# Kernel optimization log

Hardware: AMD Instinct MI355X
Metric: run time of the kernel (lower is better)

The kernel has to match this reference:

```python
import jax, jax.numpy as jnp
import numpy as np
import math

D, H, DK, DFF, B, T, K = 512, 8, 64, 2048, 8, 512, 31
P = 2 * T - 1  # rel-pos length


def _ln(x, g, b, eps=1e-5):
    mu = jnp.mean(x, -1, keepdims=True)
    var = jnp.var(x, -1, keepdims=True)
    return (x - mu) * jax.lax.rsqrt(var + eps) * g + b


def _silu(x):
    return x * jax.nn.sigmoid(x)


def _rel_shift(x):
    # x: [B,H,T,P] -> NeMo-style relative shift
    b, h, t, p = x.shape
    x = jnp.pad(x, ((0, 0), (0, 0), (0, 0), (1, 0)))
    x = x.reshape(b, h, p + 1, t)
    return x[:, :, 1:, :].reshape(b, h, t, p)


def _forward(x, pos_emb, ln1_g, ln1_b, ff1_w1, ff1_b1, ff1_w2, ff1_b2,
             lna_g, lna_b, wq, bq, wk, bk, wv, bv, wo, bo, wpos, pbu, pbv,
             lnc_g, lnc_b, pw1_w, pw1_b, dw_w, dw_b, cln_g, cln_b, pw2_w, pw2_b,
             ln2_g, ln2_b, ff2_w1, ff2_b1, ff2_w2, ff2_b2, lno_g, lno_b):
    b, t, d = x.shape
    h, dk = pbu.shape
    # FF1 (half-step residual)
    r = x
    y = _ln(x, ln1_g, ln1_b)
    y = _silu(y @ ff1_w1 + ff1_b1) @ ff1_w2 + ff1_b2
    r = r + 0.5 * y
    # Rel-pos multi-head attention
    y = _ln(r, lna_g, lna_b)
    q = (y @ wq + bq).reshape(b, t, h, dk)
    k = (y @ wk + bk).reshape(b, t, h, dk)
    v = (y @ wv + bv).reshape(b, t, h, dk)
    p = (pos_emb @ wpos).reshape(pos_emb.shape[0], -1, h, dk)[0]  # [P,H,dk]
    ac = jnp.einsum('bthd,bshd->bhts', q + pbu, k)
    bd = jnp.einsum('bthd,phd->bhtp', q + pbv, p)
    bd = _rel_shift(bd)[..., :t]
    attn = jax.nn.softmax((ac + bd) / math.sqrt(dk), axis=-1)
    o = jnp.einsum('bhts,bshd->bthd', attn, v).reshape(b, t, d) @ wo + bo
    r = r + o
    # Conformer convolution module (layer_norm variant)
    y = _ln(r, lnc_g, lnc_b)
    y = y @ pw1_w + pw1_b                       # [B,T,2D] pointwise conv1
    a, g = jnp.split(y, 2, axis=-1)
    y = a * jax.nn.sigmoid(g)                   # GLU over channels
    y = jnp.transpose(y, (0, 2, 1))             # [B,D,T]
    pad = (dw_w.shape[1] - 1) // 2
    y = jax.lax.conv_general_dilated(
        y, dw_w[:, None, :], (1,), [(pad, pad)],
        feature_group_count=d, dimension_numbers=('NCH', 'OIH', 'NCH'))
    y = y + dw_b[None, :, None]
    y = jnp.transpose(y, (0, 2, 1))             # [B,T,D]
    y = _ln(y, cln_g, cln_b)
    y = _silu(y) @ pw2_w + pw2_b                # pointwise conv2
    r = r + y
    # FF2 (half-step residual)
    y = _ln(r, ln2_g, ln2_b)
    y = _silu(y @ ff2_w1 + ff2_b1) @ ff2_w2 + ff2_b2
    r = r + 0.5 * y
    return _ln(r, lno_g, lno_b)


def setup_inputs() -> dict:
    key = jax.random.key(0)
    ks = iter(jax.random.split(key, 64))
    rn = lambda shape, s=0.05: jax.random.normal(next(ks), shape, dtype=jnp.float32) * s
    ones = lambda n: jnp.ones((n,), jnp.float32)
    zeros = lambda n: jnp.zeros((n,), jnp.float32)
    return dict(
        x=jax.random.normal(next(ks), (B, T, D), jnp.float32),
        pos_emb=jax.random.normal(next(ks), (1, P, D), jnp.float32),
        ln1_g=ones(D), ln1_b=zeros(D),
        ff1_w1=rn((D, DFF)), ff1_b1=zeros(DFF), ff1_w2=rn((DFF, D)), ff1_b2=zeros(D),
        lna_g=ones(D), lna_b=zeros(D),
        wq=rn((D, D)), bq=zeros(D), wk=rn((D, D)), bk=zeros(D),
        wv=rn((D, D)), bv=zeros(D), wo=rn((D, D)), bo=zeros(D),
        wpos=rn((D, D)), pbu=rn((H, DK)), pbv=rn((H, DK)),
        lnc_g=ones(D), lnc_b=zeros(D),
        pw1_w=rn((D, 2 * D)), pw1_b=zeros(2 * D),
        dw_w=rn((D, K)), dw_b=zeros(D),
        cln_g=ones(D), cln_b=zeros(D),
        pw2_w=rn((D, D)), pw2_b=zeros(D),
        ln2_g=ones(D), ln2_b=zeros(D),
        ff2_w1=rn((D, DFF)), ff2_b1=zeros(DFF), ff2_w2=rn((DFF, D)), ff2_b2=zeros(D),
        lno_g=ones(D), lno_b=zeros(D))


def reference(x, pos_emb, ln1_g, ln1_b, ff1_w1, ff1_b1, ff1_w2, ff1_b2,
              lna_g, lna_b, wq, bq, wk, bk, wv, bv, wo, bo, wpos, pbu, pbv,
              lnc_g, lnc_b, pw1_w, pw1_b, dw_w, dw_b, cln_g, cln_b, pw2_w, pw2_b,
              ln2_g, ln2_b, ff2_w1, ff2_b1, ff2_w2, ff2_b2, lno_g, lno_b):
    return _forward(x, pos_emb, ln1_g, ln1_b, ff1_w1, ff1_b1, ff1_w2, ff1_b2,
                    lna_g, lna_b, wq, bq, wk, bk, wv, bv, wo, bo, wpos, pbu, pbv,
                    lnc_g, lnc_b, pw1_w, pw1_b, dw_w, dw_b, cln_g, cln_b, pw2_w, pw2_b,
                    ln2_g, ln2_b, ff2_w1, ff2_b1, ff2_w2, ff2_b2, lno_g, lno_b)
```

## Files before the change

kernel.cpp:

```cpp
#include <hip/hip_runtime.h>
#include <hip/hip_bf16.h>

#define Bb 8
#define Tt 512
#define Dd 512
#define Hh 8
#define DKk 64
#define DFFf 2048
#define Pp 1023
#define KCc 31
#define BTt 4096
#define QS 1536

typedef __hip_bfloat16 bf16;
typedef __attribute__((ext_vector_type(8))) short short8;
typedef __attribute__((ext_vector_type(4))) short s4v;
typedef __attribute__((ext_vector_type(4))) float f32x4;

union BFU { __hip_bfloat16 h; short s; };
static __device__ __forceinline__ short bfbits(float f) {
    BFU u; u.h = __float2bfloat16(f); return u.s;
}
static __device__ __forceinline__ float bff(short s) {
    BFU u; u.s = s; return __bfloat162float(u.h);
}
static __device__ __forceinline__ unsigned pk2(float a, float b) {
    return (unsigned)(unsigned short)bfbits(a) | ((unsigned)(unsigned short)bfbits(b) << 16);
}

static __device__ __forceinline__ int dflag(const void* lg) {
    return ((const unsigned*)lg)[0] == 0x3F803F80u;
}

#define GLD16(g, l) __builtin_amdgcn_global_load_lds(                          \
    (const __attribute__((address_space(1))) void*)(g),                        \
    (__attribute__((address_space(3))) void*)(l), 16, 0, 0)

struct CvtDesc { const void* src; unsigned n; unsigned off; unsigned startBlk; };
struct CvtArgs { CvtDesc d[32]; };

__global__ __launch_bounds__(256) void cvt_batch_k(CvtArgs args, int ncv,
                                                   bf16* __restrict__ dst,
                                                   const void* __restrict__ lg) {
    int bid = blockIdx.x;
    int ti = 0;
    while (ti + 1 < ncv && bid >= (int)args.d[ti + 1].startBlk) ti++;
    CvtDesc de = args.d[ti];
    unsigned i = (bid - de.startBlk) * 256u + threadIdx.x;
    if (i >= de.n) return;
    float v;
    if (dflag(lg)) v = __bfloat162float(((const bf16*)de.src)[i]);
    else           v = ((const float*)de.src)[i];
    dst[de.off + i] = __float2bfloat16(v);
}

struct TD { const void* src; unsigned doff, R, C, startBlk; };
struct TArgs { TD d[11]; };

__global__ __launch_bounds__(256) void transpose_batch_k(TArgs ta, bf16* __restrict__ wt,
                                                         const void* __restrict__ lg) {
    int bid = blockIdx.x;
    int ti = 0;
    while (ti + 1 < 11 && bid >= (int)ta.d[ti + 1].startBlk) ti++;
    TD t = ta.d[ti];
    int tile = bid - t.startBlk;
    int ntc = t.C >> 5;
    int tr = tile / ntc, tc = tile % ntc;
    __shared__ short tl[32][33];
    short* out = (short*)wt + t.doff;
    int tx = threadIdx.x & 31, ty = threadIdx.x >> 5;
    int fl = dflag(lg);
#pragma unroll
    for (int i = 0; i < 32; i += 8) {
        size_t idx = (size_t)(tr * 32 + ty + i) * t.C + tc * 32 + tx;
        short v;
        if (fl) v = ((const short*)t.src)[idx];
        else    v = bfbits(((const float*)t.src)[idx]);
        tl[ty + i][tx] = v;
    }
    __syncthreads();
#pragma unroll
    for (int i = 0; i < 32; i += 8)
        out[(size_t)(tc * 32 + ty + i) * t.R + tr * 32 + tx] = tl[tx][ty + i];
}

__global__ __launch_bounds__(256) void prep_misc_k(const void* __restrict__ dww, bf16* __restrict__ dwT,
                                                   const void* __restrict__ bq, const void* __restrict__ bk,
                                                   const void* __restrict__ bv, bf16* __restrict__ bqkv,
                                                   const void* __restrict__ lg) {
    int i = blockIdx.x * 256 + threadIdx.x;
    int fl = dflag(lg);
    if (i < Dd * KCc) {
        int d = i / KCc, j = i % KCc;
        short v = fl ? ((const short*)dww)[i] : bfbits(((const float*)dww)[i]);
        ((short*)dwT)[j * Dd + d] = v;
    } else {
        int j = i - Dd * KCc;
        if (j < QS) {
            const void* s = (j < 512) ? bq : ((j < 1024) ? bk : bv);
            int idx = j & 511;
            short v = fl ? ((const short*)s)[idx] : bfbits(((const float*)s)[idx]);
            ((short*)bqkv)[j] = v;
        }
    }
}

template <int SILU>
__global__ __launch_bounds__(256) void ln_k(const float* __restrict__ in,
                                            const bf16* __restrict__ g,
                                            const bf16* __restrict__ b,
                                            bf16* __restrict__ out) {
    int row = blockIdx.x;
    int tid = threadIdx.x;
    float2 v = ((const float2*)(in + (size_t)row * Dd))[tid];
    float s = v.x + v.y;
    float ss = v.x * v.x + v.y * v.y;
#pragma unroll
    for (int off = 32; off > 0; off >>= 1) {
        s += __shfl_xor(s, off);
        ss += __shfl_xor(ss, off);
    }
    __shared__ float red[2][4];
    int wid = tid >> 6;
    if ((tid & 63) == 0) { red[0][wid] = s; red[1][wid] = ss; }
    __syncthreads();
    float S = red[0][0] + red[0][1] + red[0][2] + red[0][3];
    float SS = red[1][0] + red[1][1] + red[1][2] + red[1][3];
    float mean = S * (1.0f / Dd);
    float var = SS * (1.0f / Dd) - mean * mean;
    float rstd = rsqrtf(var + 1e-5f);
    unsigned gp = *(const unsigned*)((const short*)g + 2 * tid);
    unsigned bp = *(const unsigned*)((const short*)b + 2 * tid);
    float o0 = (v.x - mean) * rstd * bff((short)(gp & 0xFFFF)) + bff((short)(bp & 0xFFFF));
    float o1 = (v.y - mean) * rstd * bff((short)(gp >> 16)) + bff((short)(bp >> 16));
    if (SILU) {
        o0 = o0 / (1.0f + __expf(-o0));
        o1 = o1 / (1.0f + __expf(-o1));
    }
    *(unsigned*)((short*)out + (size_t)row * Dd + 2 * tid) = pk2(o0, o1);
}

__global__ __launch_bounds__(256) void ln_x_k(const void* __restrict__ x,
                                              const bf16* __restrict__ g,
                                              const bf16* __restrict__ b,
                                              float* __restrict__ r,
                                              bf16* __restrict__ out,
                                              const void* __restrict__ lg) {
    int row = blockIdx.x;
    int tid = threadIdx.x;
    size_t base = (size_t)row * Dd;
    float v0, v1;
    if (dflag(lg)) {
        unsigned xp = *(const unsigned*)((const short*)x + base + 2 * tid);
        v0 = bff((short)(xp & 0xFFFF));
        v1 = bff((short)(xp >> 16));
    } else {
        float2 xv = ((const float2*)((const float*)x + base))[tid];
        v0 = xv.x; v1 = xv.y;
    }
    ((float2*)(r + base))[tid] = make_float2(v0, v1);
    float s = v0 + v1;
    float ss = v0 * v0 + v1 * v1;
#pragma unroll
    for (int off = 32; off > 0; off >>= 1) {
        s += __shfl_xor(s, off);
        ss += __shfl_xor(ss, off);
    }
    __shared__ float red[2][4];
    int wid = tid >> 6;
    if ((tid & 63) == 0) { red[0][wid] = s; red[1][wid] = ss; }
    __syncthreads();
    float S = red[0][0] + red[0][1] + red[0][2] + red[0][3];
    float SS = red[1][0] + red[1][1] + red[1][2] + red[1][3];
    float mean = S * (1.0f / Dd);
    float var = SS * (1.0f / Dd) - mean * mean;
    float rstd = rsqrtf(var + 1e-5f);
    unsigned gp = *(const unsigned*)((const short*)g + 2 * tid);
    unsigned bp = *(const unsigned*)((const short*)b + 2 * tid);
    float o0 = (v0 - mean) * rstd * bff((short)(gp & 0xFFFF)) + bff((short)(bp & 0xFFFF));
    float o1 = (v1 - mean) * rstd * bff((short)(gp >> 16)) + bff((short)(bp >> 16));
    *(unsigned*)((short*)out + base + 2 * tid) = pk2(o0, o1);
}

__global__ __launch_bounds__(256) void ln_out_k(const float* __restrict__ in,
                                                const bf16* __restrict__ g,
                                                const bf16* __restrict__ b,
                                                void* __restrict__ out,
                                                const void* __restrict__ lg) {
    int row = blockIdx.x;
    int tid = threadIdx.x;
    size_t base = (size_t)row * Dd;
    float2 v = ((const float2*)(in + base))[tid];
    float s = v.x + v.y;
    float ss = v.x * v.x + v.y * v.y;
#pragma unroll
    for (int off = 32; off > 0; off >>= 1) {
        s += __shfl_xor(s, off);
        ss += __shfl_xor(ss, off);
    }
    __shared__ float red[2][4];
    int wid = tid >> 6;
    if ((tid & 63) == 0) { red[0][wid] = s; red[1][wid] = ss; }
    __syncthreads();
    float S = red[0][0] + red[0][1] + red[0][2] + red[0][3];
    float SS = red[1][0] + red[1][1] + red[1][2] + red[1][3];
    float mean = S * (1.0f / Dd);
    float var = SS * (1.0f / Dd) - mean * mean;
    float rstd = rsqrtf(var + 1e-5f);
    unsigned gp = *(const unsigned*)((const short*)g + 2 * tid);
    unsigned bp = *(const unsigned*)((const short*)b + 2 * tid);
    float o0 = (v.x - mean) * rstd * bff((short)(gp & 0xFFFF)) + bff((short)(bp & 0xFFFF));
    float o1 = (v.y - mean) * rstd * bff((short)(gp >> 16)) + bff((short)(bp >> 16));
    if (dflag(lg)) {
        *(unsigned*)((short*)out + base + 2 * tid) = pk2(o0, o1);
    } else {
        ((float2*)((float*)out + base))[tid] = make_float2(o0, o1);
    }
}

template <int BM, int BN, int BK, int WM, int WN, typename CT, int ACT, int RES, int VT>
__global__ __launch_bounds__(256) void gemm_mfma_k(const bf16* __restrict__ Abf,
                                                   const bf16* __restrict__ WT,
                                                   const bf16* __restrict__ bias,
                                                   const float* __restrict__ resid,
                                                   CT* __restrict__ C,
                                                   bf16* __restrict__ vt,
                                                   int M, int N, int Kd, float alpha) {
    constexpr int MT = WM / 16, NT = WN / 16;
    constexpr int WX = BN / WN;
    constexpr int CPB = BK / 8;
    constexpr int KS = BK / 32;
    __shared__ __align__(16) short As[BM * BK];
    __shared__ __align__(16) short Bs[BN * BK];
    int tid = threadIdx.x;
    int wid = tid >> 6, lane = tid & 63;
    int lm = lane & 15, quad = lane >> 4;
    int wy = wid / WX, wx = wid % WX;
    int bm = blockIdx.y * BM, bn = blockIdx.x * BN;
    const short* Ag = (const short*)Abf;
    const short* Bg = (const short*)WT;

    f32x4 acc[MT][NT] = {};

    for (int k0 = 0; k0 < Kd; k0 += BK) {
#pragma unroll
        for (int it = 0; it < BM * CPB / 256; it++) {
            int c = it * 256 + tid;
            int row = c / CPB;
            int q = (c % CPB) ^ (row & 7);
            int gr = bm + row;
            if (gr > M - 1) gr = M - 1;
            GLD16(Ag + (size_t)gr * Kd + k0 + q * 8, As + (it * 256 + wid * 64) * 8);
        }
#pragma unroll
        for (int it = 0; it < BN * CPB / 256; it++) {
            int c = it * 256 + tid;
            int row = c / CPB;
            int q = (c % CPB) ^ (row & 7);
            GLD16(Bg + (size_t)(bn + row) * Kd + k0 + q * 8, Bs + (it * 256 + wid * 64) * 8);
        }
        __syncthreads();
        short8 af[MT][KS], bfv[NT][KS];
#pragma unroll
        for (int mt = 0; mt < MT; mt++) {
            int row = wy * WM + mt * 16 + lm;
#pragma unroll
            for (int ks = 0; ks < KS; ks++)
                af[mt][ks] = *(const short8*)&As[row * BK + (((ks * 4 + quad) ^ (row & 7)) * 8)];
        }
#pragma unroll
        for (int nt = 0; nt < NT; nt++) {
            int row = wx * WN + nt * 16 + lm;
#pragma unroll
            for (int ks = 0; ks < KS; ks++)
                bfv[nt][ks] = *(const short8*)&Bs[row * BK + (((ks * 4 + quad) ^ (row & 7)) * 8)];
        }
#pragma unroll
        for (int ks = 0; ks < KS; ks++)
#pragma unroll
            for (int mt = 0; mt < MT; mt++)
#pragma unroll
                for (int nt = 0; nt < NT; nt++)
                    acc[mt][nt] = __builtin_amdgcn_mfma_f32_16x16x32_bf16(af[mt][ks], bfv[nt][ks], acc[mt][nt], 0, 0, 0);
        __syncthreads();
    }

#pragma unroll
    for (int mt = 0; mt < MT; mt++) {
#pragma unroll
        for (int nt = 0; nt < NT; nt++) {
            int gcol = bn + wx * WN + nt * 16 + lm;
            int growb = bm + wy * WM + mt * 16 + quad * 4;
            if (VT && gcol >= 1024) {
                float bi = bias ? __bfloat162float(bias[gcol]) : 0.f;
                s4v pk;
#pragma unroll
                for (int r = 0; r < 4; r++) pk[r] = bfbits(acc[mt][nt][r] + bi);
                *(s4v*)((short*)vt + (size_t)((growb >> 9) * 512 + (gcol - 1024)) * 512 + (growb & 511)) = pk;
            } else {
#pragma unroll
                for (int r = 0; r < 4; r++) {
                    int grow = growb + r;
                    if (grow >= M) continue;
                    float v = acc[mt][nt][r];
                    if (bias) v += __bfloat162float(bias[gcol]);
                    if (ACT == 1) v = v / (1.0f + __expf(-v));
                    if (RES == 1) v = resid[(size_t)grow * N + gcol] + alpha * v;
                    C[(size_t)grow * N + gcol] = (CT)v;
                }
            }
        }
    }
}

__global__ __launch_bounds__(256) void gemm_glu_k(const bf16* __restrict__ Abf,
                                                  const bf16* __restrict__ WT,
                                                  const bf16* __restrict__ bias,
                                                  bf16* __restrict__ C) {
    constexpr int BM = 64, BN = 64, BK = 64, WM = 32, WN = 32;
    constexpr int MT = WM / 16, NT = WN / 16, WX = BN / WN, CPB = BK / 8, KS = BK / 32;
    __shared__ __align__(16) short As[BM * BK];
    __shared__ __align__(16) short Bs[2 * BN * BK];
    int tid = threadIdx.x;
    int wid = tid >> 6, lane = tid & 63;
    int lm = lane & 15, quad = lane >> 4;
    int wy = wid / WX, wx = wid % WX;
    int bm = blockIdx.y * BM, bn = blockIdx.x * BN;
    const short* Ag = (const short*)Abf;
    const short* Bg = (const short*)WT;

    f32x4 acc[MT][NT][2] = {};

    for (int k0 = 0; k0 < Dd; k0 += BK) {
#pragma unroll
        for (int it = 0; it < BM * CPB / 256; it++) {
            int c = it * 256 + tid;
            int row = c / CPB;
            int q = (c % CPB) ^ (row & 7);
            GLD16(Ag + (size_t)(bm + row) * Dd + k0 + q * 8, As + (it * 256 + wid * 64) * 8);
        }
#pragma unroll
        for (int it = 0; it < 2 * BN * CPB / 256; it++) {
            int c = it * 256 + tid;
            int row = c / CPB;
            int q = (c % CPB) ^ (row & 7);
            int wrow = (row < BN) ? (bn + row) : (512 + bn + row - BN);
            GLD16(Bg + (size_t)wrow * Dd + k0 + q * 8, Bs + (it * 256 + wid * 64) * 8);
        }
        __syncthreads();
        short8 af[MT][KS], bfv[NT][2][KS];
#pragma unroll
        for (int mt = 0; mt < MT; mt++) {
            int row = wy * WM + mt * 16 + lm;
#pragma unroll
            for (int ks = 0; ks < KS; ks++)
                af[mt][ks] = *(const short8*)&As[row * BK + (((ks * 4 + quad) ^ (row & 7)) * 8)];
        }
#pragma unroll
        for (int nt = 0; nt < NT; nt++) {
#pragma unroll
            for (int hf = 0; hf < 2; hf++) {
                int row = hf * BN + wx * WN + nt * 16 + lm;
#pragma unroll
                for (int ks = 0; ks < KS; ks++)
                    bfv[nt][hf][ks] = *(const short8*)&Bs[row * BK + (((ks * 4 + quad) ^ (row & 7)) * 8)];
            }
        }
#pragma unroll
        for (int ks = 0; ks < KS; ks++)
#pragma unroll
            for (int mt = 0; mt < MT; mt++)
#pragma unroll
                for (int nt = 0; nt < NT; nt++) {
                    acc[mt][nt][0] = __builtin_amdgcn_mfma_f32_16x16x32_bf16(af[mt][ks], bfv[nt][0][ks], acc[mt][nt][0], 0, 0, 0);
                    acc[mt][nt][1] = __builtin_amdgcn_mfma_f32_16x16x32_bf16(af[mt][ks], bfv[nt][1][ks], acc[mt][nt][1], 0, 0, 0);
                }
        __syncthreads();
    }

#pragma unroll
    for (int mt = 0; mt < MT; mt++) {
#pragma unroll
        for (int nt = 0; nt < NT; nt++) {
#pragma unroll
            for (int r = 0; r < 4; r++) {
                int grow = bm + wy * WM + mt * 16 + quad * 4 + r;
                int gcol = bn + wx * WN + nt * 16 + lm;
                float va = acc[mt][nt][0][r] + __bfloat162float(bias[gcol]);
                float vg = acc[mt][nt][1][r] + __bfloat162float(bias[512 + gcol]);
                float v = va / (1.0f + __expf(-vg));
                C[(size_t)grow * Dd + gcol] = __float2bfloat16(v);
            }
        }
    }
}

#define PST 520

__global__ __launch_bounds__(256, 4) void attn_mfma_k(const bf16* __restrict__ qkv,
                                                      const bf16* __restrict__ p,
                                                      const bf16* __restrict__ vT,
                                                      const bf16* __restrict__ pbu,
                                                      const bf16* __restrict__ pbv,
                                                      bf16* __restrict__ out) {
    __shared__ __align__(16) short Pl[16 * PST];
    __shared__ __align__(16) float redm[16][4];
    __shared__ __align__(16) float reds[16][4];
    int tid = threadIdx.x;
    int wid = tid >> 6;
    int lane = tid & 63;
    int lm = lane & 15;
    int quad = lane >> 4;
    int bidx = (blockIdx.x & 7) * 256 + (blockIdx.x >> 3);
    int b = bidx >> 8;
    int h = (bidx >> 5) & 7;
    int t0 = (bidx & 31) * 16;

    const short* qkvs = (const short*)qkv;
    const short* ps = (const short*)p;

    short8 qu[2], qv[2];
    {
        size_t rowbase = ((size_t)(b * Tt + t0 + lm) * QS) + h * DKk;
        const short* pbus = (const short*)pbu + h * DKk + quad * 8;
        const short* pbvs = (const short*)pbv + h * DKk + quad * 8;
#pragma unroll
        for (int ksp = 0; ksp < 2; ksp++) {
            short8 raw = *(const short8*)(qkvs + rowbase + ksp * 32 + quad * 8);
            short8 bu = *(const short8*)(pbus + ksp * 32);
            short8 bv = *(const short8*)(pbvs + ksp * 32);
#pragma unroll
            for (int j = 0; j < 8; j++) {
                float qf = bff(raw[j]);
                qu[ksp][j] = bfbits(qf + bff(bu[j]));
                qv[ksp][j] = bfbits(qf + bff(bv[j]));
            }
        }
    }

    const float scale = 0.125f;
    int pb0 = 511 - t0 + wid * 128;

    f32x4 dprev = {0.f, 0.f, 0.f, 0.f};
    {
        int prow = pb0 - 16 + lm;
        if (prow < 0) prow = 0;
        const short* pa = ps + (size_t)prow * Dd + h * DKk + quad * 8;
        dprev = __builtin_amdgcn_mfma_f32_16x16x32_bf16(qv[0], *(const short8*)pa, dprev, 0, 0, 0);
        dprev = __builtin_amdgcn_mfma_f32_16x16x32_bf16(qv[1], *(const short8*)(pa + 32), dprev, 0, 0, 0);
    }

    f32x4 sreg[8];
#pragma unroll
    for (int i = 0; i < 8; i++) {
        int st = wid * 8 + i;
        f32x4 ac = {0.f, 0.f, 0.f, 0.f};
        f32x4 dcur = {0.f, 0.f, 0.f, 0.f};
        const short* ka = qkvs + ((size_t)(b * Tt + st * 16 + lm) * QS) + 512 + h * DKk + quad * 8;
        const short* pa = ps + (size_t)(pb0 + i * 16 + lm) * Dd + h * DKk + quad * 8;
        ac = __builtin_amdgcn_mfma_f32_16x16x32_bf16(qu[0], *(const short8*)ka, ac, 0, 0, 0);
        ac = __builtin_amdgcn_mfma_f32_16x16x32_bf16(qu[1], *(const short8*)(ka + 32), ac, 0, 0, 0);
        dcur = __builtin_amdgcn_mfma_f32_16x16x32_bf16(qv[0], *(const short8*)pa, dcur, 0, 0, 0);
        dcur = __builtin_amdgcn_mfma_f32_16x16x32_bf16(qv[1], *(const short8*)(pa + 32), dcur, 0, 0, 0);
#pragma unroll
        for (int r = 0; r < 4; r++) {
            int m = quad * 4 + r;
            int j = (lm - m) & 15;
            int srcl = quad * 16 + j;
            float b2 = __shfl(dcur[r], srcl, 64);
            float b1 = __shfl(dprev[r], srcl, 64);
            float bd = (lm >= m) ? b2 : b1;
            sreg[i][r] = scale * (ac[r] + bd);
        }
        dprev = dcur;
    }

    float mrow[4];
#pragma unroll
    for (int r = 0; r < 4; r++) {
        float m = sreg[0][r];
#pragma unroll
        for (int i = 1; i < 8; i++) m = fmaxf(m, sreg[i][r]);
#pragma unroll
        for (int off = 1; off < 16; off <<= 1) m = fmaxf(m, __shfl_xor(m, off));
        mrow[r] = m;
    }
    if (lm < 4) {
        float v = (lm == 0) ? mrow[0] : (lm == 1) ? mrow[1] : (lm == 2) ? mrow[2] : mrow[3];
        redm[quad * 4 + lm][wid] = v;
    }
    __syncthreads();

    float gm[4], srow[4];
#pragma unroll
    for (int r = 0; r < 4; r++) {
        float4 mv = *(const float4*)&redm[quad * 4 + r][0];
        gm[r] = fmaxf(fmaxf(mv.x, mv.y), fmaxf(mv.z, mv.w));
        srow[r] = 0.f;
    }
#pragma unroll
    for (int i = 0; i < 8; i++) {
        int col = (wid * 8 + i) * 16 + lm;
#pragma unroll
        for (int r = 0; r < 4; r++) {
            float e = __expf(sreg[i][r] - gm[r]);
            srow[r] += e;
            Pl[(quad * 4 + r) * PST + col] = bfbits(e);
        }
    }
#pragma unroll
    for (int r = 0; r < 4; r++) {
#pragma unroll
        for (int off = 1; off < 16; off <<= 1) srow[r] += __shfl_xor(srow[r], off);
    }
    if (lm < 4) {
        float v = (lm == 0) ? srow[0] : (lm == 1) ? srow[1] : (lm == 2) ? srow[2] : srow[3];
        reds[quad * 4 + lm][wid] = v;
    }
    __syncthreads();

    float lsum[4];
#pragma unroll
    for (int r = 0; r < 4; r++) {
        float4 sv = *(const float4*)&reds[quad * 4 + r][0];
        lsum[r] = (sv.x + sv.y) + (sv.z + sv.w);
    }

    int d0 = wid * 16;
    const short* vrow = (const short*)vT + ((size_t)(b * Hh + h) * DKk + d0 + lm) * Tt;
    const short* parow = Pl + (size_t)lm * PST;
    f32x4 o0 = {0.f, 0.f, 0.f, 0.f};
    f32x4 o1 = {0.f, 0.f, 0.f, 0.f};
#pragma unroll
    for (int ksp = 0; ksp < 16; ksp += 2) {
        short8 a0 = *(const short8*)(parow + ksp * 32 + quad * 8);
        short8 v0 = *(const short8*)(vrow + ksp * 32 + quad * 8);
        short8 a1 = *(const short8*)(parow + (ksp + 1) * 32 + quad * 8);
        short8 v1 = *(const short8*)(vrow + (ksp + 1) * 32 + quad * 8);
        o0 = __builtin_amdgcn_mfma_f32_16x16x32_bf16(a0, v0, o0, 0, 0, 0);
        o1 = __builtin_amdgcn_mfma_f32_16x16x32_bf16(a1, v1, o1, 0, 0, 0);
    }
    f32x4 o = o0 + o1;
    short* os = (short*)out;
#pragma unroll
    for (int r = 0; r < 4; r++) {
        int m = quad * 4 + r;
        os[((size_t)(b * Tt + t0 + m) * Dd) + h * DKk + d0 + lm] = bfbits(o[r] / lsum[r]);
    }
}

__global__ __launch_bounds__(256) void dwconv_ln_k(const bf16* __restrict__ in,
                                                   const bf16* __restrict__ wT,
                                                   const bf16* __restrict__ bdw,
                                                   const bf16* __restrict__ g,
                                                   const bf16* __restrict__ bb,
                                                   bf16* __restrict__ out) {
    int row = blockIdx.x * 4 + (threadIdx.x >> 6);
    int lane = threadIdx.x & 63;
    int d0 = lane * 8;
    int t = row & 511, b = row >> 9;
    const short* ins = (const short*)in + (size_t)b * Tt * Dd;
    const short* wts = (const short*)wT;
    float acc[8];
    short8 bv = *(const short8*)((const short*)bdw + d0);
#pragma unroll
    for (int e = 0; e < 8; e++) acc[e] = bff(bv[e]);
#pragma unroll
    for (int j = 0; j < KCc; j++) {
        int tt = t + j - 15;
        if (tt < 0 || tt >= Tt) continue;
        short8 iv = *(const short8*)(ins + (size_t)tt * Dd + d0);
        short8 wv = *(const short8*)(wts + j * Dd + d0);
#pragma unroll
        for (int e = 0; e < 8; e++) acc[e] += bff(iv[e]) * bff(wv[e]);
    }
    float s = 0.f, ss = 0.f;
#pragma unroll
    for (int e = 0; e < 8; e++) { s += acc[e]; ss += acc[e] * acc[e]; }
#pragma unroll
    for (int off = 32; off > 0; off >>= 1) {
        s += __shfl_xor(s, off);
        ss += __shfl_xor(ss, off);
    }
    float mean = s * (1.0f / Dd);
    float var = ss * (1.0f / Dd) - mean * mean;
    float rstd = rsqrtf(var + 1e-5f);
    short8 gv = *(const short8*)((const short*)g + d0);
    short8 bbv = *(const short8*)((const short*)bb + d0);
    short8 ov;
#pragma unroll
    for (int e = 0; e < 8; e++) {
        float o = (acc[e] - mean) * rstd * bff(gv[e]) + bff(bbv[e]);
        o = o / (1.0f + __expf(-o));
        ov[e] = bfbits(o);
    }
    *(short8*)((short*)out + (size_t)row * Dd + d0) = ov;
}

extern "C" void kernel_launch(void* const* d_in, const int* in_sizes, int n_in,
                              void* d_out, int out_size, void* d_ws, size_t ws_size,
                              hipStream_t stream) {
    char* base = (char*)d_ws;
    bf16* wb = (bf16*)(base + 256);

    size_t woff[39];
    size_t acc = 0;
    for (int i = 1; i < 39; i++) { woff[i] = acc; acc += (size_t)in_sizes[i]; }
    size_t wbytes = (2 * acc + 255) & ~(size_t)255;

    const size_t NBT = (size_t)BTt * Dd;
    float* r   = (float*)((char*)wb + wbytes);
    bf16* a    = (bf16*)((char*)r + NBT * 4);
    bf16* big  = a + NBT;
    bf16* pbuf = big + (size_t)BTt * DFFf;
    bf16* wt   = pbuf + (size_t)Pp * Dd;

    const void* lg = d_in[2];

    bf16* c_pos   = wb + woff[1];
    bf16* c_ln1g  = wb + woff[2],  *c_ln1b = wb + woff[3];
    bf16* c_f1b1  = wb + woff[5];
    bf16* c_f1b2  = wb + woff[7];
    bf16* c_lnag  = wb + woff[8],  *c_lnab = wb + woff[9];
    bf16* c_bo    = wb + woff[17];
    bf16* c_pbu   = wb + woff[19], *c_pbv  = wb + woff[20];
    bf16* c_lncg  = wb + woff[21], *c_lncb = wb + woff[22];
    bf16* c_p1b   = wb + woff[24];
    bf16* c_dwb   = wb + woff[26];
    bf16* c_clng  = wb + woff[27], *c_clnb = wb + woff[28];
    bf16* c_p2b   = wb + woff[30];
    bf16* c_ln2g  = wb + woff[31], *c_ln2b = wb + woff[32];
    bf16* c_f2b1  = wb + woff[34];
    bf16* c_f2b2  = wb + woff[36];
    bf16* c_lnog  = wb + woff[37], *c_lnob = wb + woff[38];

    const int tin[11]  = {4, 6, 10, 12, 14, 16, 18, 23, 29, 33, 35};
    const unsigned tR[11] = {512, 2048, 512, 512, 512, 512, 512, 512, 512, 512, 2048};
    const unsigned tC[11] = {2048, 512, 512, 512, 512, 512, 512, 1024, 512, 2048, 512};
    size_t toff[11]; size_t tacc = 0;
    for (int i = 0; i < 11; i++) { toff[i] = tacc; tacc += (size_t)tR[i] * tC[i]; }
    bf16* t_f1w1 = wt + toff[0];
    bf16* t_f1w2 = wt + toff[1];
    bf16* t_wqkv = wt + toff[2];
    bf16* t_wo   = wt + toff[5];
    bf16* t_wpos = wt + toff[6];
    bf16* t_p1w  = wt + toff[7];
    bf16* t_p2w  = wt + toff[8];
    bf16* t_f2w1 = wt + toff[9];
    bf16* t_f2w2 = wt + toff[10];
    bf16* bias_qkv = wt + tacc;
    bf16* dwT      = bias_qkv + QS;
    bf16* vTb      = dwT + KCc * Dd;

    dim3 blk(256);

    bool skip[39] = {};
    for (int i = 0; i < 11; i++) skip[tin[i]] = true;
    skip[11] = skip[13] = skip[15] = skip[25] = true;
    CvtArgs ca;
    int ncv = 0;
    unsigned blkacc = 0;
    for (int i = 1; i < 39; i++) {
        if (skip[i]) continue;
        ca.d[ncv].src = d_in[i];
        ca.d[ncv].n = (unsigned)in_sizes[i];
        ca.d[ncv].off = (unsigned)woff[i];
        ca.d[ncv].startBlk = blkacc;
        blkacc += (unsigned)((in_sizes[i] + 255) / 256);
        ncv++;
    }
    cvt_batch_k<<<blkacc, blk, 0, stream>>>(ca, ncv, wb, lg);

    TArgs ta;
    unsigned tblk = 0;
    for (int i = 0; i < 11; i++) {
        ta.d[i].src = d_in[tin[i]];
        ta.d[i].doff = (unsigned)toff[i];
        ta.d[i].R = tR[i];
        ta.d[i].C = tC[i];
        ta.d[i].startBlk = tblk;
        tblk += (tR[i] >> 5) * (tC[i] >> 5);
    }
    transpose_batch_k<<<tblk, blk, 0, stream>>>(ta, wt, lg);
    prep_misc_k<<<(Dd * KCc + QS + 255) / 256, blk, 0, stream>>>(
        d_in[25], dwT, d_in[11], d_in[13], d_in[15], bias_qkv, lg);

    auto g128 = [](int M, int N) { return dim3(N / 128, M / 128); };
    auto g64  = [](int M, int N) { return dim3(N / 64, (M + 63) / 64); };

    ln_x_k<<<BTt, blk, 0, stream>>>(d_in[0], c_ln1g, c_ln1b, r, a, lg);
    gemm_mfma_k<128, 128, 64, 64, 64, bf16, 1, 0, 0><<<g128(BTt, DFFf), blk, 0, stream>>>(
        a, t_f1w1, c_f1b1, nullptr, big, nullptr, BTt, DFFf, Dd, 0.f);
    gemm_mfma_k<64, 64, 128, 32, 32, float, 0, 1, 0><<<g64(BTt, Dd), blk, 0, stream>>>(
        big, t_f1w2, c_f1b2, r, r, nullptr, BTt, Dd, DFFf, 0.5f);

    bf16* qkvb = big;
    bf16* cb   = big + 3 * NBT;
    ln_k<0><<<BTt, blk, 0, stream>>>(r, c_lnag, c_lnab, a);
    gemm_mfma_k<128, 64, 64, 64, 32, bf16, 0, 0, 1><<<dim3(QS / 64, BTt / 128), blk, 0, stream>>>(
        a, t_wqkv, bias_qkv, nullptr, qkvb, vTb, BTt, QS, Dd, 0.f);
    gemm_mfma_k<64, 64, 64, 32, 32, bf16, 0, 0, 0><<<g64(Pp, Dd), blk, 0, stream>>>(
        c_pos, t_wpos, nullptr, nullptr, pbuf, nullptr, Pp, Dd, Dd, 0.f);
    attn_mfma_k<<<Bb * Hh * (Tt / 16), blk, 0, stream>>>(qkvb, pbuf, vTb, c_pbu, c_pbv, cb);
    gemm_mfma_k<64, 64, 64, 32, 32, float, 0, 1, 0><<<g64(BTt, Dd), blk, 0, stream>>>(
        cb, t_wo, c_bo, r, r, nullptr, BTt, Dd, Dd, 1.0f);

    bf16* gluo = big + 2 * NBT;
    ln_k<0><<<BTt, blk, 0, stream>>>(r, c_lncg, c_lncb, a);
    gemm_glu_k<<<dim3(Dd / 64, BTt / 64), blk, 0, stream>>>(a, t_p1w, c_p1b, gluo);
    dwconv_ln_k<<<BTt / 4, blk, 0, stream>>>(gluo, dwT, c_dwb, c_clng, c_clnb, a);
    gemm_mfma_k<64, 64, 64, 32, 32, float, 0, 1, 0><<<g64(BTt, Dd), blk, 0, stream>>>(
        a, t_p2w, c_p2b, r, r, nullptr, BTt, Dd, Dd, 1.0f);

    ln_k<0><<<BTt, blk, 0, stream>>>(r, c_ln2g, c_ln2b, a);
    gemm_mfma_k<128, 128, 64, 64, 64, bf16, 1, 0, 0><<<g128(BTt, DFFf), blk, 0, stream>>>(
        a, t_f2w1, c_f2b1, nullptr, big, nullptr, BTt, DFFf, Dd, 0.f);
    gemm_mfma_k<64, 64, 128, 32, 32, float, 0, 1, 0><<<g64(BTt, Dd), blk, 0, stream>>>(
        big, t_f2w2, c_f2b2, r, r, nullptr, BTt, Dd, DFFf, 0.5f);

    ln_out_k<<<BTt, blk, 0, stream>>>(r, c_lnog, c_lnob, d_out, lg);
}
```

Baseline: 430.3 us.

## Store K, V, and positional projections in MFMA fragment-order layouts for attention

The QKV GEMM epilogue now writes K and V into layouts arranged in MFMA operand fragment order. A new prep kernel reorders the positional projection into a per-head fragment layout, including a zero block for the shifted boundary. The attention kernel then loads each operand as contiguous 16-byte-per-lane reads instead of strided row gathers across the 1536-wide QKV buffer. In exchange there is an extra small kernel launch, and the K epilogue does scattered 2-byte stores that may be slow.

```diff
diff --git a/kernel.cpp b/kernel.cpp
--- a/kernel.cpp
+++ b/kernel.cpp
@@ -105,6 +105,24 @@
     }
 }
 
+__global__ __launch_bounds__(256) void prep_pf_k(const bf16* __restrict__ pbuf,
+                                                 bf16* __restrict__ pF) {
+    int h = blockIdx.x >> 6, J = blockIdx.x & 63;
+    int idx = threadIdx.x * 4;
+    int ksp = idx >> 9;
+    int l = (idx >> 3) & 63;
+    int e0 = idx & 7;
+    int lm = l & 15, qd = l >> 4;
+    int prow = J * 16 - 1 + lm;
+    s4v v;
+    if (prow < 0) {
+        v = s4v{0, 0, 0, 0};
+    } else {
+        v = *(const s4v*)((const short*)pbuf + (size_t)prow * Dd + h * DKk + ksp * 32 + qd * 8 + e0);
+    }
+    *(s4v*)((short*)pF + ((size_t)h * 64 + J) * 1024 + idx) = v;
+}
+
 template <int SILU>
 __global__ __launch_bounds__(256) void ln_k(const float* __restrict__ in,
                                             const bf16* __restrict__ g,
@@ -225,6 +243,7 @@
                                                    const float* __restrict__ resid,
                                                    CT* __restrict__ C,
                                                    bf16* __restrict__ vt,
+                                                   bf16* __restrict__ kf,
                                                    int M, int N, int Kd, float alpha) {
     constexpr int MT = WM / 16, NT = WN / 16;
     constexpr int WX = BN / WN;
@@ -292,11 +311,27 @@
             int gcol = bn + wx * WN + nt * 16 + lm;
             int growb = bm + wy * WM + mt * 16 + quad * 4;
             if (VT && gcol >= 1024) {
+                int hd = gcol - 1024;
+                int h = hd >> 6, d = hd & 63;
+                int b = growb >> 9, tt = growb & 511;
                 float bi = bias ? __bfloat162float(bias[gcol]) : 0.f;
                 s4v pk;
 #pragma unroll
                 for (int r = 0; r < 4; r++) pk[r] = bfbits(acc[mt][nt][r] + bi);
-                *(s4v*)((short*)vt + (size_t)((growb >> 9) * 512 + (gcol - 1024)) * 512 + (growb & 511)) = pk;
+                size_t base = (((((size_t)b * 8 + h) * 16 + (tt >> 5)) * 4 + (d >> 4)) * 64 +
+                               (((tt >> 3) & 3) * 16 + (d & 15))) * 8 + (tt & 7);
+                *(s4v*)((short*)vt + base) = pk;
+            } else if (VT && gcol >= 512) {
+                int hd = gcol - 512;
+                int h = hd >> 6, kk = hd & 63;
+                int b = growb >> 9, tt = growb & 511;
+                float bi = __bfloat162float(bias[gcol]);
+                size_t base2 = ((((size_t)b * 8 + h) * 32 + (tt >> 4)) * 2 + (kk >> 5)) * 512;
+                int qd = (kk >> 3) & 3, e = kk & 7;
+#pragma unroll
+                for (int r = 0; r < 4; r++)
+                    ((short*)kf)[base2 + (size_t)(qd * 16 + (tt & 15) + r) * 8 + e] =
+                        bfbits(acc[mt][nt][r] + bi);
             } else {
 #pragma unroll
                 for (int r = 0; r < 4; r++) {
@@ -398,8 +433,9 @@
 #define PST 520
 
 __global__ __launch_bounds__(256, 4) void attn_mfma_k(const bf16* __restrict__ qkv,
-                                                      const bf16* __restrict__ p,
-                                                      const bf16* __restrict__ vT,
+                                                      const bf16* __restrict__ kF,
+                                                      const bf16* __restrict__ pF,
+                                                      const bf16* __restrict__ vF,
                                                       const bf16* __restrict__ pbu,
                                                       const bf16* __restrict__ pbv,
                                                       bf16* __restrict__ out) {
@@ -417,7 +453,6 @@
     int t0 = (bidx & 31) * 16;
 
     const short* qkvs = (const short*)qkv;
-    const short* ps = (const short*)p;
 
     short8 qu[2], qv[2];
     {
@@ -439,15 +474,15 @@
     }
 
     const float scale = 0.125f;
-    int pb0 = 511 - t0 + wid * 128;
+    const short* kFs = (const short*)kF + ((size_t)(b * 8 + h) * 32) * 1024;
+    const short* pFs = (const short*)pF + ((size_t)h * 64) * 1024;
+    int Jbase = 32 - (t0 >> 4) + wid * 8;
 
     f32x4 dprev = {0.f, 0.f, 0.f, 0.f};
     {
-        int prow = pb0 - 16 + lm;
-        if (prow < 0) prow = 0;
-        const short* pa = ps + (size_t)prow * Dd + h * DKk + quad * 8;
+        const short* pa = pFs + (size_t)(Jbase - 1) * 1024 + lane * 8;
         dprev = __builtin_amdgcn_mfma_f32_16x16x32_bf16(qv[0], *(const short8*)pa, dprev, 0, 0, 0);
-        dprev = __builtin_amdgcn_mfma_f32_16x16x32_bf16(qv[1], *(const short8*)(pa + 32), dprev, 0, 0, 0);
+        dprev = __builtin_amdgcn_mfma_f32_16x16x32_bf16(qv[1], *(const short8*)(pa + 512), dprev, 0, 0, 0);
     }
 
     f32x4 sreg[8];
@@ -456,12 +491,12 @@
         int st = wid * 8 + i;
         f32x4 ac = {0.f, 0.f, 0.f, 0.f};
         f32x4 dcur = {0.f, 0.f, 0.f, 0.f};
-        const short* ka = qkvs + ((size_t)(b * Tt + st * 16 + lm) * QS) + 512 + h * DKk + quad * 8;
-        const short* pa = ps + (size_t)(pb0 + i * 16 + lm) * Dd + h * DKk + quad * 8;
+        const short* ka = kFs + (size_t)st * 1024 + lane * 8;
+        const short* pa = pFs + (size_t)(Jbase + i) * 1024 + lane * 8;
         ac = __builtin_amdgcn_mfma_f32_16x16x32_bf16(qu[0], *(const short8*)ka, ac, 0, 0, 0);
-        ac = __builtin_amdgcn_mfma_f32_16x16x32_bf16(qu[1], *(const short8*)(ka + 32), ac, 0, 0, 0);
+        ac = __builtin_amdgcn_mfma_f32_16x16x32_bf16(qu[1], *(const short8*)(ka + 512), ac, 0, 0, 0);
         dcur = __builtin_amdgcn_mfma_f32_16x16x32_bf16(qv[0], *(const short8*)pa, dcur, 0, 0, 0);
-        dcur = __builtin_amdgcn_mfma_f32_16x16x32_bf16(qv[1], *(const short8*)(pa + 32), dcur, 0, 0, 0);
+        dcur = __builtin_amdgcn_mfma_f32_16x16x32_bf16(qv[1], *(const short8*)(pa + 512), dcur, 0, 0, 0);
 #pragma unroll
         for (int r = 0; r < 4; r++) {
             int m = quad * 4 + r;
@@ -527,16 +562,16 @@
     }
 
     int d0 = wid * 16;
-    const short* vrow = (const short*)vT + ((size_t)(b * Hh + h) * DKk + d0 + lm) * Tt;
+    const short* va = (const short*)vF + (size_t)(b * 8 + h) * 32768 + wid * 512 + lane * 8;
     const short* parow = Pl + (size_t)lm * PST;
     f32x4 o0 = {0.f, 0.f, 0.f, 0.f};
     f32x4 o1 = {0.f, 0.f, 0.f, 0.f};
 #pragma unroll
     for (int ksp = 0; ksp < 16; ksp += 2) {
         short8 a0 = *(const short8*)(parow + ksp * 32 + quad * 8);
-        short8 v0 = *(const short8*)(vrow + ksp * 32 + quad * 8);
+        short8 v0 = *(const short8*)(va + (size_t)ksp * 2048);
         short8 a1 = *(const short8*)(parow + (ksp + 1) * 32 + quad * 8);
-        short8 v1 = *(const short8*)(vrow + (ksp + 1) * 32 + quad * 8);
+        short8 v1 = *(const short8*)(va + (size_t)(ksp + 1) * 2048);
         o0 = __builtin_amdgcn_mfma_f32_16x16x32_bf16(a0, v0, o0, 0, 0, 0);
         o1 = __builtin_amdgcn_mfma_f32_16x16x32_bf16(a1, v1, o1, 0, 0, 0);
     }
@@ -651,6 +686,8 @@
     bf16* bias_qkv = wt + tacc;
     bf16* dwT      = bias_qkv + QS;
     bf16* vTb      = dwT + KCc * Dd;
+    bf16* kFb      = vTb + (size_t)2097152;
+    bf16* pFb      = kFb + (size_t)2097152;
 
     dim3 blk(256);
 
@@ -690,33 +727,34 @@
 
     ln_x_k<<<BTt, blk, 0, stream>>>(d_in[0], c_ln1g, c_ln1b, r, a, lg);
     gemm_mfma_k<128, 128, 64, 64, 64, bf16, 1, 0, 0><<<g128(BTt, DFFf), blk, 0, stream>>>(
-        a, t_f1w1, c_f1b1, nullptr, big, nullptr, BTt, DFFf, Dd, 0.f);
+        a, t_f1w1, c_f1b1, nullptr, big, nullptr, nullptr, BTt, DFFf, Dd, 0.f);
     gemm_mfma_k<64, 64, 128, 32, 32, float, 0, 1, 0><<<g64(BTt, Dd), blk, 0, stream>>>(
-        big, t_f1w2, c_f1b2, r, r, nullptr, BTt, Dd, DFFf, 0.5f);
+        big, t_f1w2, c_f1b2, r, r, nullptr, nullptr, BTt, Dd, DFFf, 0.5f);
 
     bf16* qkvb = big;
     bf16* cb   = big + 3 * NBT;
     ln_k<0><<<BTt, blk, 0, stream>>>(r, c_lnag, c_lnab, a);
     gemm_mfma_k<128, 64, 64, 64, 32, bf16, 0, 0, 1><<<dim3(QS / 64, BTt / 128), blk, 0, stream>>>(
-        a, t_wqkv, bias_qkv, nullptr, qkvb, vTb, BTt, QS, Dd, 0.f);
+        a, t_wqkv, bias_qkv, nullptr, qkvb, vTb, kFb, BTt, QS, Dd, 0.f);
     gemm_mfma_k<64, 64, 64, 32, 32, bf16, 0, 0, 0><<<g64(Pp, Dd), blk, 0, stream>>>(
-        c_pos, t_wpos, nullptr, nullptr, pbuf, nullptr, Pp, Dd, Dd, 0.f);
-    attn_mfma_k<<<Bb * Hh * (Tt / 16), blk, 0, stream>>>(qkvb, pbuf, vTb, c_pbu, c_pbv, cb);
+        c_pos, t_wpos, nullptr, nullptr, pbuf, nullptr, nullptr, Pp, Dd, Dd, 0.f);
+    prep_pf_k<<<8 * 64, blk, 0, stream>>>(pbuf, pFb);
+    attn_mfma_k<<<Bb * Hh * (Tt / 16), blk, 0, stream>>>(qkvb, kFb, pFb, vTb, c_pbu, c_pbv, cb);
     gemm_mfma_k<64, 64, 64, 32, 32, float, 0, 1, 0><<<g64(BTt, Dd), blk, 0, stream>>>(
-        cb, t_wo, c_bo, r, r, nullptr, BTt, Dd, Dd, 1.0f);
+        cb, t_wo, c_bo, r, r, nullptr, nullptr, BTt, Dd, Dd, 1.0f);
 
     bf16* gluo = big + 2 * NBT;
     ln_k<0><<<BTt, blk, 0, stream>>>(r, c_lncg, c_lncb, a);
     gemm_glu_k<<<dim3(Dd / 64, BTt / 64), blk, 0, stream>>>(a, t_p1w, c_p1b, gluo);
     dwconv_ln_k<<<BTt / 4, blk, 0, stream>>>(gluo, dwT, c_dwb, c_clng, c_clnb, a);
     gemm_mfma_k<64, 64, 64, 32, 32, float, 0, 1, 0><<<g64(BTt, Dd), blk, 0, stream>>>(
-        a, t_p2w, c_p2b, r, r, nullptr, BTt, Dd, Dd, 1.0f);
+        a, t_p2w, c_p2b, r, r, nullptr, nullptr, BTt, Dd, Dd, 1.0f);
 
     ln_k<0><<<BTt, blk, 0, stream>>>(r, c_ln2g, c_ln2b, a);
     gemm_mfma_k<128, 128, 64, 64, 64, bf16, 1, 0, 0><<<g128(BTt, DFFf), blk, 0, stream>>>(
-        a, t_f2w1, c_f2b1, nullptr, big, nullptr, BTt, DFFf, Dd, 0.f);
+        a, t_f2w1, c_f2b1, nullptr, big, nullptr, nullptr, BTt, DFFf, Dd, 0.f);
     gemm_mfma_k<64, 64, 128, 32, 32, float, 0, 1, 0><<<g64(BTt, Dd), blk, 0, stream>>>(
-        big, t_f2w2, c_f2b2, r, r, nullptr, BTt, Dd, DFFf, 0.5f);
+        big, t_f2w2, c_f2b2, r, r, nullptr, nullptr, BTt, Dd, DFFf, 0.5f);
 
     ln_out_k<<<BTt, blk, 0, stream>>>(r, c_lnog, c_lnob, d_out, lg);
 }
```

After: 411.0 us. 1.05x faster.
